# Kernel tuning notes

Measured on AMD Instinct MI355X. Metric: run time of the kernel, lower is better.

## Reference

```python
import jax, jax.numpy as jnp
import numpy as np

N = 50000      # nodes
E = 800000     # edges (undirected, stored once)
D_IN = 128
D_OUT = 128


def setup_inputs() -> dict:
    key = jax.random.key(0)
    k1, k2, k3, k4 = jax.random.split(key, 4)
    X = jax.random.normal(k1, (N, D_IN), dtype=jnp.float32)
    edges = jax.random.randint(k2, (E, 2), 0, N, dtype=jnp.int32)
    weights = jax.random.uniform(k3, (E,), dtype=jnp.float32)
    # glorot_uniform kernel W: [D_IN, D_OUT]
    limit = np.sqrt(6.0 / (D_IN + D_OUT)).astype(np.float32)
    W = jax.random.uniform(k4, (D_IN, D_OUT), dtype=jnp.float32, minval=-limit, maxval=limit)
    return {"X": X, "edges": edges, "weights": weights, "W": W}


def reference(X, edges, weights, W):
    # D^{-1} @ A @ X @ W with A the symmetric weighted adjacency from the edge list.
    # nx.Graph is undirected -> each edge contributes in both directions.
    src = jnp.concatenate([edges[:, 0], edges[:, 1]])   # [2E]
    dst = jnp.concatenate([edges[:, 1], edges[:, 0]])   # [2E]
    w = jnp.concatenate([weights, weights])             # [2E]
    # (A @ X)[i] = sum over edges (j -> i) of w * X[j]
    ax = jax.ops.segment_sum(w[:, None] * X[src], dst, num_segments=N)  # [N, D_IN]
    deg = jax.ops.segment_sum(w, dst, num_segments=N)                   # [N]
    inv_deg = jnp.where(deg > 0, 1.0 / deg, 0.0)                        # D^{-1} (safe for isolated nodes)
    return (ax * inv_deg[:, None]) @ W                                  # [N, D_OUT]
```

## Files before the change

kernel.cpp:

```cpp
#include <hip/hip_runtime.h>
#include <hip/hip_fp16.h>

#define NN 50000
#define NE 800000
#define D  128
#define NB 391
#define NS 256
#define EPS 3125
#define SN (NB * NS)
#define SCB 1024
#define NSB ((SN + SCB - 1) / SCB)

#define OFF_SLAB 0
#define OFF_XW   0
#define OFF_CSR4 12800000
#define OFF_HIST 19200000
#define OFF_BASE 19600384
#define OFF_BSUM 20000768
#define OFF_ROW  20001280
#define OFF_WF   20201344
#define NEED_A   20234112

#define OFF_CNT  0
#define OFF_ROWF 200704
#define OFF_CUR  401408
#define OFF_CSR8 602112

typedef float v2f  __attribute__((ext_vector_type(2)));
typedef __attribute__((ext_vector_type(8))) short bf16x8;
typedef __attribute__((ext_vector_type(4))) float f32x4;

__device__ __forceinline__ float bf_lo(unsigned int v) { return __uint_as_float(v << 16); }
__device__ __forceinline__ float bf_hi(unsigned int v) { return __uint_as_float(v & 0xffff0000u); }
__device__ __forceinline__ float wdec(unsigned int v) {
    return __half2float(__ushort_as_half((unsigned short)(v >> 16)));
}
__device__ __forceinline__ unsigned short bf16rne(float f) {
    unsigned int b = __float_as_uint(f);
    return (unsigned short)((b + 0x7fffu + ((b >> 16) & 1u)) >> 16);
}

__global__ __launch_bounds__(256) void gc_shist(
    const int2* __restrict__ edges, int* __restrict__ histT)
{
    __shared__ int h[NB];
    const int s = blockIdx.x;
    for (int i = threadIdx.x; i < NB; i += 256) h[i] = 0;
    __syncthreads();
    const int e0 = s * EPS;
    for (int i = threadIdx.x; i < EPS; i += 256) {
        int2 p = edges[e0 + i];
        atomicAdd(&h[p.y >> 7], 1);
        atomicAdd(&h[p.x >> 7], 1);
    }
    __syncthreads();
    for (int b = threadIdx.x; b < NB; b += 256) histT[b * NS + s] = h[b];
}

__global__ __launch_bounds__(256) void gc_scanA(
    const int* __restrict__ in, int* __restrict__ bsum)
{
    __shared__ int red[256];
    int base = blockIdx.x * SCB;
    int s = 0;
    for (int i = threadIdx.x; i < SCB; i += 256) {
        int idx = base + i;
        s += (idx < SN) ? in[idx] : 0;
    }
    red[threadIdx.x] = s;
    __syncthreads();
    for (int off = 128; off > 0; off >>= 1) {
        if (threadIdx.x < off) red[threadIdx.x] += red[threadIdx.x + off];
        __syncthreads();
    }
    if (threadIdx.x == 0) bsum[blockIdx.x] = red[0];
}

__global__ __launch_bounds__(256) void gc_scanC(
    const int* __restrict__ in, const int* __restrict__ bsum,
    int* __restrict__ baseT)
{
    __shared__ int part[256];
    __shared__ int sb[128];
    const int t = threadIdx.x;

    int own = 0;
    if (t < 128) {
        own = (t < NSB) ? bsum[t] : 0;
        sb[t] = own;
    }
    __syncthreads();
    for (int off = 1; off < 128; off <<= 1) {
        int v = (t < 128 && t >= off) ? sb[t - off] : 0;
        __syncthreads();
        if (t < 128) sb[t] += v;
        __syncthreads();
    }
    __shared__ int bexc;
    if (t == (int)blockIdx.x) bexc = sb[t] - own;
    __syncthreads();

    int base = blockIdx.x * SCB;
    int idx0 = base + t * 4;
    int4 v = make_int4(0, 0, 0, 0);
    if (idx0 + 3 < SN) v = *reinterpret_cast<const int4*>(in + idx0);
    int s = v.x + v.y + v.z + v.w;
    part[t] = s;
    __syncthreads();
    for (int off = 1; off < 256; off <<= 1) {
        int x = (t >= off) ? part[t - off] : 0;
        __syncthreads();
        part[t] += x;
        __syncthreads();
    }
    int run = bexc + part[t] - s;
    if (idx0 + 3 < SN)
        *reinterpret_cast<int4*>(baseT + idx0) =
            make_int4(run, run + v.x, run + v.x + v.y, run + v.x + v.y + v.z);
}

__global__ __launch_bounds__(256) void gc_sscat(
    const int2* __restrict__ edges, const float* __restrict__ wts,
    const int* __restrict__ baseT, int2* __restrict__ slab)
{
    __shared__ int cur[NB];
    const int s = blockIdx.x;
    for (int b = threadIdx.x; b < NB; b += 256) cur[b] = baseT[b * NS + s];
    __syncthreads();
    const int e0 = s * EPS;
    for (int i = threadIdx.x; i < EPS; i += 256) {
        int2 p = edges[e0 + i];
        int wb = __float_as_int(wts[e0 + i]);
        int b = p.y >> 7;
        int pos = atomicAdd(&cur[b], 1);
        slab[pos] = make_int2(p.x | ((p.y & 127) << 16), wb);
        b = p.x >> 7;
        pos = atomicAdd(&cur[b], 1);
        slab[pos] = make_int2(p.y | ((p.x & 127) << 16), wb);
    }
}

__global__ __launch_bounds__(256) void gc_csr(
    const int* __restrict__ baseT, const int2* __restrict__ slab,
    int* __restrict__ row_start, unsigned int* __restrict__ csr4)
{
    __shared__ int ncnt[128], ncur[128], part[128];
    const int tid = threadIdx.x;
    const int b = blockIdx.x;
    const int start = baseT[b * NS];
    const int end = (b == NB - 1) ? (2 * NE) : baseT[(b + 1) * NS];

    if (tid < 128) ncnt[tid] = 0;
    __syncthreads();

    for (int j = start + tid; j < end; j += 256)
        atomicAdd(&ncnt[(slab[j].x >> 16) & 127], 1);
    __syncthreads();

    if (tid < 128) part[tid] = ncnt[tid];
    __syncthreads();
    for (int off = 1; off < 128; off <<= 1) {
        int v = 0;
        if (tid < 128 && tid >= off) v = part[tid - off];
        __syncthreads();
        if (tid < 128) part[tid] += v;
        __syncthreads();
    }
    if (tid < 128) {
        int st = start + part[tid] - ncnt[tid];
        int n = b * 128 + tid;
        if (n < NN) row_start[n] = st;
        ncur[tid] = st;
    }
    if (b == 0 && tid == 0) row_start[NN] = 2 * NE;
    __syncthreads();

    for (int j = start + tid; j < end; j += 256) {
        int2 en = slab[j];
        int dl = (en.x >> 16) & 127;
        unsigned int hb =
            (unsigned int)__half_as_ushort(__float2half_rn(__int_as_float(en.y))) << 16;
        int pos = atomicAdd(&ncur[dl], 1);
        csr4[pos] = (unsigned int)(en.x & 0xffff) | hb;
    }
}

__global__ __launch_bounds__(256) void gc_wfrag(
    const float* __restrict__ Wm, unsigned short* __restrict__ wf)
{
    int t = blockIdx.x * 256 + threadIdx.x;
    int j    = t & 7;
    int lane = (t >> 3) & 63;
    int nt   = (t >> 9) & 7;
    int ki   = t >> 12;
    int k = ki * 32 + (lane >> 4) * 8 + j;
    int n = nt * 16 + (lane & 15);
    wf[t] = bf16rne(Wm[k * D + n]);
}

__global__ __launch_bounds__(256) void gc_gemm_mfma(
    const float* __restrict__ X, const unsigned short* __restrict__ wf,
    unsigned short* __restrict__ dst)
{
    const int lane = threadIdx.x & 63;
    const int wave = threadIdx.x >> 6;
    const int rbase = blockIdx.x * 64 + wave * 16;
    const int r  = lane & 15;
    const int kb = lane >> 4;

    f32x4 acc[8];
    #pragma unroll
    for (int i = 0; i < 8; ++i) acc[i] = f32x4{0.f, 0.f, 0.f, 0.f};

    const bf16x8* wfv = reinterpret_cast<const bf16x8*>(wf);
    const int row = rbase + r;
    const bool rok = row < NN;

    #pragma unroll
    for (int ki = 0; ki < 4; ++ki) {
        float4 a0 = make_float4(0.f, 0.f, 0.f, 0.f);
        float4 a1 = make_float4(0.f, 0.f, 0.f, 0.f);
        if (rok) {
            const float4* xp = reinterpret_cast<const float4*>(
                X + (size_t)row * D + ki * 32 + kb * 8);
            a0 = xp[0];
            a1 = xp[1];
        }
        bf16x8 af;
        af[0] = (short)bf16rne(a0.x); af[1] = (short)bf16rne(a0.y);
        af[2] = (short)bf16rne(a0.z); af[3] = (short)bf16rne(a0.w);
        af[4] = (short)bf16rne(a1.x); af[5] = (short)bf16rne(a1.y);
        af[6] = (short)bf16rne(a1.z); af[7] = (short)bf16rne(a1.w);
        #pragma unroll
        for (int nt = 0; nt < 8; ++nt) {
            bf16x8 bf = wfv[(ki * 8 + nt) * 64 + lane];
            acc[nt] = __builtin_amdgcn_mfma_f32_16x16x32_bf16(af, bf, acc[nt], 0, 0, 0);
        }
    }

    const int orow0 = rbase + kb * 4;
    #pragma unroll
    for (int nt = 0; nt < 8; ++nt) {
        #pragma unroll
        for (int reg = 0; reg < 4; ++reg) {
            int orow = orow0 + reg;
            if (orow < NN)
                dst[(size_t)orow * D + nt * 16 + r] = bf16rne(acc[nt][reg]);
        }
    }
}

__global__ __launch_bounds__(256) void gc_gather4(
    const int* __restrict__ row_start, const unsigned int* __restrict__ csr4,
    const unsigned int* __restrict__ F, float* __restrict__ out)
{
    int wid  = (blockIdx.x * 256 + threadIdx.x) >> 6;
    unsigned int lane = threadIdx.x & 63;
    if (wid >= NN) return;
    int j   = row_start[wid];
    int end = row_start[wid + 1];
    v2f acc = {0.f, 0.f};
    float dw = 0.f;
    for (; j + 16 <= end; j += 16) {
        unsigned int e[16], v[16];
        #pragma unroll
        for (int q = 0; q < 16; ++q) e[q] = csr4[j + q];
        #pragma unroll
        for (int q = 0; q < 16; ++q) v[q] = F[((e[q] & 0xffffu) << 6) | lane];
        #pragma unroll
        for (int q = 0; q < 16; ++q) {
            float w = wdec(e[q]);
            acc += w * v2f{bf_lo(v[q]), bf_hi(v[q])};
            dw += w;
        }
    }
    for (; j + 4 <= end; j += 4) {
        unsigned int e0 = csr4[j],     e1 = csr4[j + 1];
        unsigned int e2 = csr4[j + 2], e3 = csr4[j + 3];
        unsigned int v0 = F[((e0 & 0xffffu) << 6) | lane];
        unsigned int v1 = F[((e1 & 0xffffu) << 6) | lane];
        unsigned int v2 = F[((e2 & 0xffffu) << 6) | lane];
        unsigned int v3 = F[((e3 & 0xffffu) << 6) | lane];
        float w0 = wdec(e0), w1 = wdec(e1), w2 = wdec(e2), w3 = wdec(e3);
        acc += w0 * v2f{bf_lo(v0), bf_hi(v0)};
        acc += w1 * v2f{bf_lo(v1), bf_hi(v1)};
        acc += w2 * v2f{bf_lo(v2), bf_hi(v2)};
        acc += w3 * v2f{bf_lo(v3), bf_hi(v3)};
        dw += (w0 + w1) + (w2 + w3);
    }
    for (; j < end; ++j) {
        unsigned int e0 = csr4[j];
        unsigned int v0 = F[((e0 & 0xffffu) << 6) | lane];
        float w0 = wdec(e0);
        acc += w0 * v2f{bf_lo(v0), bf_hi(v0)};
        dw += w0;
    }
    float inv = dw > 0.f ? 1.f / dw : 0.f;
    float2 r; r.x = acc.x * inv; r.y = acc.y * inv;
    reinterpret_cast<float2*>(out)[(size_t)wid * 64 + lane] = r;
}

__global__ __launch_bounds__(256) void gc_hist(
    const int2* __restrict__ edges, int* __restrict__ counts)
{
    int e = blockIdx.x * 256 + threadIdx.x;
    if (e >= NE) return;
    int2 p = edges[e];
    atomicAdd(counts + p.x, 1);
    atomicAdd(counts + p.y, 1);
}

__global__ __launch_bounds__(1024) void gc_scan(
    const int* __restrict__ counts, int* __restrict__ row_start,
    int* __restrict__ cursor)
{
    const int CHUNK = (NN + 1023) / 1024;
    __shared__ int part[1024];
    int t = threadIdx.x;
    int lo = t * CHUNK, hi = min(lo + CHUNK, NN);
    int s = 0;
    for (int i = lo; i < hi; ++i) s += counts[i];
    part[t] = s;
    __syncthreads();
    for (int off = 1; off < 1024; off <<= 1) {
        int v = (t >= off) ? part[t - off] : 0;
        __syncthreads();
        part[t] += v;
        __syncthreads();
    }
    int run = part[t] - s;
    for (int i = lo; i < hi; ++i) {
        int c = counts[i];
        row_start[i] = run;
        cursor[i]    = run;
        run += c;
    }
    if (t == 1023) row_start[NN] = part[1023];
}

__global__ __launch_bounds__(256) void gc_fill8(
    const int2* __restrict__ edges, const float* __restrict__ wts,
    int* __restrict__ cursor, int2* __restrict__ csr)
{
    int e = blockIdx.x * 256 + threadIdx.x;
    if (e >= NE) return;
    int2 p = edges[e];
    int wb = __float_as_int(wts[e]);
    int pos = atomicAdd(cursor + p.y, 1);
    csr[pos] = make_int2(p.x, wb);
    pos = atomicAdd(cursor + p.x, 1);
    csr[pos] = make_int2(p.y, wb);
}

__global__ __launch_bounds__(256) void gc_gather_f32(
    const int* __restrict__ row_start, const int2* __restrict__ csr,
    const float* __restrict__ F, float* __restrict__ out)
{
    int wid  = (blockIdx.x * 256 + threadIdx.x) >> 6;
    int lane = threadIdx.x & 63;
    if (wid >= NN) return;
    int j   = row_start[wid];
    int end = row_start[wid + 1];
    const float2* F2 = reinterpret_cast<const float2*>(F);
    float ax = 0.f, ay = 0.f, dw = 0.f;
    for (; j < end; ++j) {
        int2  cw = csr[j];
        float w  = __int_as_float(cw.y);
        float2 xv = F2[(size_t)cw.x * 64 + lane];
        ax = fmaf(w, xv.x, ax);
        ay = fmaf(w, xv.y, ay);
        dw += w;
    }
    float inv = dw > 0.f ? 1.f / dw : 0.f;
    float2 r; r.x = ax * inv; r.y = ay * inv;
    reinterpret_cast<float2*>(out)[(size_t)wid * 64 + lane] = r;
}

__global__ __launch_bounds__(256) void gc_gemm_f32(
    const float* __restrict__ src, float* __restrict__ dst,
    const float* __restrict__ Wm)
{
    __shared__ float Ws[D * D];
    __shared__ float axs[16 * D];
    const int tid = threadIdx.x;
    const int col = tid & 127;
    const int ty  = tid >> 7;
    const int rbase = blockIdx.x * 16;

    const float4* W4  = reinterpret_cast<const float4*>(Wm);
    float4*       Ws4 = reinterpret_cast<float4*>(Ws);
    #pragma unroll
    for (int i = 0; i < 16; ++i) Ws4[tid + i * 256] = W4[tid + i * 256];

    const float4* A4   = reinterpret_cast<const float4*>(src + (size_t)rbase * D);
    float4*       axs4 = reinterpret_cast<float4*>(axs);
    #pragma unroll
    for (int i = 0; i < 2; ++i) axs4[tid + i * 256] = A4[tid + i * 256];
    __syncthreads();

    float acc[8];
    #pragma unroll
    for (int i = 0; i < 8; ++i) acc[i] = 0.f;

    for (int k = 0; k < D; ++k) {
        float wv = Ws[k * D + col];
        #pragma unroll
        for (int i = 0; i < 8; ++i)
            acc[i] = fmaf(axs[(ty * 8 + i) * D + k], wv, acc[i]);
    }

    #pragma unroll
    for (int i = 0; i < 8; ++i)
        dst[(size_t)(rbase + ty * 8 + i) * D + col] = acc[i];
}

extern "C" void kernel_launch(void* const* d_in, const int* in_sizes, int n_in,
                              void* d_out, int out_size, void* d_ws, size_t ws_size,
                              hipStream_t stream) {
    const float* X     = (const float*)d_in[0];
    const int2*  edges = (const int2*)d_in[1];
    const float* wts   = (const float*)d_in[2];
    const float* Wm    = (const float*)d_in[3];
    float* out = (float*)d_out;
    char*  ws  = (char*)d_ws;

    const int eblocks = (NE + 255) / 256;

    if (ws_size >= NEED_A) {
        int2* slab  = (int2*)(ws + OFF_SLAB);
        unsigned int* csr4 = (unsigned int*)(ws + OFF_CSR4);
        int*  histT = (int*)(ws + OFF_HIST);
        int*  baseT = (int*)(ws + OFF_BASE);
        int*  bsum  = (int*)(ws + OFF_BSUM);
        int*  row   = (int*)(ws + OFF_ROW);
        unsigned short* wf = (unsigned short*)(ws + OFF_WF);
        unsigned short* xw = (unsigned short*)(ws + OFF_XW);

        gc_shist<<<NS, 256, 0, stream>>>(edges, histT);
        gc_scanA<<<NSB, 256, 0, stream>>>(histT, bsum);
        gc_scanC<<<NSB, 256, 0, stream>>>(histT, bsum, baseT);
        gc_sscat<<<NS, 256, 0, stream>>>(edges, wts, baseT, slab);
        gc_wfrag<<<64, 256, 0, stream>>>(Wm, wf);
        gc_csr<<<NB, 256, 0, stream>>>(baseT, slab, row, csr4);
        gc_gemm_mfma<<<(NN + 63) / 64, 256, 0, stream>>>(X, wf, xw);
        gc_gather4<<<(NN * 64 + 255) / 256, 256, 0, stream>>>(
            row, csr4, (const unsigned int*)xw, out);
    } else {
        int*  counts    = (int*) (ws + OFF_CNT);
        int*  row_start = (int*) (ws + OFF_ROWF);
        int*  cursor    = (int*) (ws + OFF_CUR);
        int2* csr       = (int2*)(ws + OFF_CSR8);

        hipMemsetAsync(counts, 0, NN * sizeof(int), stream);
        gc_hist<<<eblocks, 256, 0, stream>>>(edges, counts);
        gc_scan<<<1, 1024, 0, stream>>>(counts, row_start, cursor);
        gc_fill8<<<eblocks, 256, 0, stream>>>(edges, wts, cursor, csr);
        gc_gather_f32<<<(NN * 64 + 255) / 256, 256, 0, stream>>>(row_start, csr, X, out);
        gc_gemm_f32<<<NN / 16, 256, 0, stream>>>(out, out, Wm);
    }
}
```

Measured before the change: 108.9 us.

## Fuse CSR build kernels into one cooperative kernel with grid syncs

Merges the six graph-build launches (histogram, two scan phases, scatter, W fragment packing, per-bucket CSR) into a single cooperative kernel of 391 blocks separated by grid-wide barriers. The aim is to remove per-launch overhead and inter-kernel gaps on a short, launch-bound pipeline. The cost is that phases with few active blocks leave most of the grid idle, and each grid.sync adds its own barrier latency. Cooperative launch also needs every block resident at once, which 391 blocks of 256 threads should meet on this GPU.

```diff
diff --git a/kernel.cpp b/kernel.cpp
--- a/kernel.cpp
+++ b/kernel.cpp
@@ -1,5 +1,8 @@
 #include <hip/hip_runtime.h>
 #include <hip/hip_fp16.h>
+#include <hip/hip_cooperative_groups.h>
+
+namespace cg = cooperative_groups;
 
 #define NN 50000
 #define NE 800000
@@ -40,162 +43,157 @@
     return (unsigned short)((b + 0x7fffu + ((b >> 16) & 1u)) >> 16);
 }
 
-__global__ __launch_bounds__(256) void gc_shist(
-    const int2* __restrict__ edges, int* __restrict__ histT)
-{
+__global__ __launch_bounds__(256) void gc_build(
+    const int2* __restrict__ edges, const float* __restrict__ wts,
+    const float* __restrict__ Wm, int* __restrict__ histT,
+    int* __restrict__ bsum, int* __restrict__ baseT,
+    int2* __restrict__ slab, int* __restrict__ row_start,
+    unsigned int* __restrict__ csr4, unsigned short* __restrict__ wf)
+{
+    cg::grid_group grid = cg::this_grid();
     __shared__ int h[NB];
-    const int s = blockIdx.x;
-    for (int i = threadIdx.x; i < NB; i += 256) h[i] = 0;
-    __syncthreads();
-    const int e0 = s * EPS;
-    for (int i = threadIdx.x; i < EPS; i += 256) {
-        int2 p = edges[e0 + i];
-        atomicAdd(&h[p.y >> 7], 1);
-        atomicAdd(&h[p.x >> 7], 1);
-    }
-    __syncthreads();
-    for (int b = threadIdx.x; b < NB; b += 256) histT[b * NS + s] = h[b];
-}
-
-__global__ __launch_bounds__(256) void gc_scanA(
-    const int* __restrict__ in, int* __restrict__ bsum)
-{
-    __shared__ int red[256];
-    int base = blockIdx.x * SCB;
-    int s = 0;
-    for (int i = threadIdx.x; i < SCB; i += 256) {
-        int idx = base + i;
-        s += (idx < SN) ? in[idx] : 0;
-    }
-    red[threadIdx.x] = s;
-    __syncthreads();
-    for (int off = 128; off > 0; off >>= 1) {
-        if (threadIdx.x < off) red[threadIdx.x] += red[threadIdx.x + off];
-        __syncthreads();
-    }
-    if (threadIdx.x == 0) bsum[blockIdx.x] = red[0];
-}
-
-__global__ __launch_bounds__(256) void gc_scanC(
-    const int* __restrict__ in, const int* __restrict__ bsum,
-    int* __restrict__ baseT)
-{
     __shared__ int part[256];
     __shared__ int sb[128];
-    const int t = threadIdx.x;
-
-    int own = 0;
-    if (t < 128) {
-        own = (t < NSB) ? bsum[t] : 0;
-        sb[t] = own;
-    }
-    __syncthreads();
-    for (int off = 1; off < 128; off <<= 1) {
-        int v = (t < 128 && t >= off) ? sb[t - off] : 0;
-        __syncthreads();
-        if (t < 128) sb[t] += v;
-        __syncthreads();
-    }
-    __shared__ int bexc;
-    if (t == (int)blockIdx.x) bexc = sb[t] - own;
-    __syncthreads();
-
-    int base = blockIdx.x * SCB;
-    int idx0 = base + t * 4;
-    int4 v = make_int4(0, 0, 0, 0);
-    if (idx0 + 3 < SN) v = *reinterpret_cast<const int4*>(in + idx0);
-    int s = v.x + v.y + v.z + v.w;
-    part[t] = s;
-    __syncthreads();
-    for (int off = 1; off < 256; off <<= 1) {
-        int x = (t >= off) ? part[t - off] : 0;
-        __syncthreads();
-        part[t] += x;
-        __syncthreads();
-    }
-    int run = bexc + part[t] - s;
-    if (idx0 + 3 < SN)
-        *reinterpret_cast<int4*>(baseT + idx0) =
-            make_int4(run, run + v.x, run + v.x + v.y, run + v.x + v.y + v.z);
-}
-
-__global__ __launch_bounds__(256) void gc_sscat(
-    const int2* __restrict__ edges, const float* __restrict__ wts,
-    const int* __restrict__ baseT, int2* __restrict__ slab)
-{
-    __shared__ int cur[NB];
-    const int s = blockIdx.x;
-    for (int b = threadIdx.x; b < NB; b += 256) cur[b] = baseT[b * NS + s];
-    __syncthreads();
-    const int e0 = s * EPS;
-    for (int i = threadIdx.x; i < EPS; i += 256) {
-        int2 p = edges[e0 + i];
-        int wb = __float_as_int(wts[e0 + i]);
-        int b = p.y >> 7;
-        int pos = atomicAdd(&cur[b], 1);
-        slab[pos] = make_int2(p.x | ((p.y & 127) << 16), wb);
-        b = p.x >> 7;
-        pos = atomicAdd(&cur[b], 1);
-        slab[pos] = make_int2(p.y | ((p.x & 127) << 16), wb);
-    }
-}
-
-__global__ __launch_bounds__(256) void gc_csr(
-    const int* __restrict__ baseT, const int2* __restrict__ slab,
-    int* __restrict__ row_start, unsigned int* __restrict__ csr4)
-{
-    __shared__ int ncnt[128], ncur[128], part[128];
+    __shared__ int bexc_s;
+    __shared__ int ncnt[128], ncur[128];
+
     const int tid = threadIdx.x;
-    const int b = blockIdx.x;
-    const int start = baseT[b * NS];
-    const int end = (b == NB - 1) ? (2 * NE) : baseT[(b + 1) * NS];
-
-    if (tid < 128) ncnt[tid] = 0;
-    __syncthreads();
-
-    for (int j = start + tid; j < end; j += 256)
-        atomicAdd(&ncnt[(slab[j].x >> 16) & 127], 1);
-    __syncthreads();
-
-    if (tid < 128) part[tid] = ncnt[tid];
-    __syncthreads();
-    for (int off = 1; off < 128; off <<= 1) {
-        int v = 0;
-        if (tid < 128 && tid >= off) v = part[tid - off];
-        __syncthreads();
-        if (tid < 128) part[tid] += v;
-        __syncthreads();
-    }
-    if (tid < 128) {
-        int st = start + part[tid] - ncnt[tid];
-        int n = b * 128 + tid;
-        if (n < NN) row_start[n] = st;
-        ncur[tid] = st;
-    }
-    if (b == 0 && tid == 0) row_start[NN] = 2 * NE;
-    __syncthreads();
-
-    for (int j = start + tid; j < end; j += 256) {
-        int2 en = slab[j];
-        int dl = (en.x >> 16) & 127;
-        unsigned int hb =
-            (unsigned int)__half_as_ushort(__float2half_rn(__int_as_float(en.y))) << 16;
-        int pos = atomicAdd(&ncur[dl], 1);
-        csr4[pos] = (unsigned int)(en.x & 0xffff) | hb;
-    }
-}
-
-__global__ __launch_bounds__(256) void gc_wfrag(
-    const float* __restrict__ Wm, unsigned short* __restrict__ wf)
-{
-    int t = blockIdx.x * 256 + threadIdx.x;
-    int j    = t & 7;
-    int lane = (t >> 3) & 63;
-    int nt   = (t >> 9) & 7;
-    int ki   = t >> 12;
-    int k = ki * 32 + (lane >> 4) * 8 + j;
-    int n = nt * 16 + (lane & 15);
-    wf[t] = bf16rne(Wm[k * D + n]);
+    const int bid = blockIdx.x;
+
+    if (bid < NS) {
+        const int s = bid;
+        for (int i = tid; i < NB; i += 256) h[i] = 0;
+        __syncthreads();
+        const int e0 = s * EPS;
+        for (int i = tid; i < EPS; i += 256) {
+            int2 p = edges[e0 + i];
+            atomicAdd(&h[p.y >> 7], 1);
+            atomicAdd(&h[p.x >> 7], 1);
+        }
+        __syncthreads();
+        for (int b = tid; b < NB; b += 256) histT[b * NS + s] = h[b];
+    } else if (bid < NS + 64) {
+        int t = (bid - NS) * 256 + tid;
+        int j    = t & 7;
+        int lane = (t >> 3) & 63;
+        int nt   = (t >> 9) & 7;
+        int ki   = t >> 12;
+        int k = ki * 32 + (lane >> 4) * 8 + j;
+        int n = nt * 16 + (lane & 15);
+        wf[t] = bf16rne(Wm[k * D + n]);
+    }
+    grid.sync();
+
+    if (bid < NSB) {
+        int base = bid * SCB;
+        int s = 0;
+        for (int i = tid; i < SCB; i += 256) {
+            int idx = base + i;
+            s += (idx < SN) ? histT[idx] : 0;
+        }
+        part[tid] = s;
+        __syncthreads();
+        for (int off = 128; off > 0; off >>= 1) {
+            if (tid < off) part[tid] += part[tid + off];
+            __syncthreads();
+        }
+        if (tid == 0) bsum[bid] = part[0];
+    }
+    grid.sync();
+
+    if (bid < NSB) {
+        int own = 0;
+        if (tid < 128) {
+            own = (tid < NSB) ? bsum[tid] : 0;
+            sb[tid] = own;
+        }
+        __syncthreads();
+        for (int off = 1; off < 128; off <<= 1) {
+            int v = (tid < 128 && tid >= off) ? sb[tid - off] : 0;
+            __syncthreads();
+            if (tid < 128) sb[tid] += v;
+            __syncthreads();
+        }
+        if (tid == bid) bexc_s = sb[tid] - own;
+        __syncthreads();
+
+        int base = bid * SCB;
+        int idx0 = base + tid * 4;
+        int4 v = make_int4(0, 0, 0, 0);
+        if (idx0 + 3 < SN) v = *reinterpret_cast<const int4*>(histT + idx0);
+        int s = v.x + v.y + v.z + v.w;
+        part[tid] = s;
+        __syncthreads();
+        for (int off = 1; off < 256; off <<= 1) {
+            int x = (tid >= off) ? part[tid - off] : 0;
+            __syncthreads();
+            part[tid] += x;
+            __syncthreads();
+        }
+        int run = bexc_s + part[tid] - s;
+        if (idx0 + 3 < SN)
+            *reinterpret_cast<int4*>(baseT + idx0) =
+                make_int4(run, run + v.x, run + v.x + v.y, run + v.x + v.y + v.z);
+    }
+    grid.sync();
+
+    if (bid < NS) {
+        const int s = bid;
+        for (int b = tid; b < NB; b += 256) h[b] = baseT[b * NS + s];
+        __syncthreads();
+        const int e0 = s * EPS;
+        for (int i = tid; i < EPS; i += 256) {
+            int2 p = edges[e0 + i];
+            int wb = __float_as_int(wts[e0 + i]);
+            int b = p.y >> 7;
+            int pos = atomicAdd(&h[b], 1);
+            slab[pos] = make_int2(p.x | ((p.y & 127) << 16), wb);
+            b = p.x >> 7;
+            pos = atomicAdd(&h[b], 1);
+            slab[pos] = make_int2(p.y | ((p.x & 127) << 16), wb);
+        }
+    }
+    grid.sync();
+
+    {
+        const int b = bid;
+        const int start = baseT[b * NS];
+        const int end = (b == NB - 1) ? (2 * NE) : baseT[(b + 1) * NS];
+
+        if (tid < 128) ncnt[tid] = 0;
+        __syncthreads();
+
+        for (int j = start + tid; j < end; j += 256)
+            atomicAdd(&ncnt[(slab[j].x >> 16) & 127], 1);
+        __syncthreads();
+
+        if (tid < 128) part[tid] = ncnt[tid];
+        __syncthreads();
+        for (int off = 1; off < 128; off <<= 1) {
+            int v = 0;
+            if (tid < 128 && tid >= off) v = part[tid - off];
+            __syncthreads();
+            if (tid < 128) part[tid] += v;
+            __syncthreads();
+        }
+        if (tid < 128) {
+            int st = start + part[tid] - ncnt[tid];
+            int n = b * 128 + tid;
+            if (n < NN) row_start[n] = st;
+            ncur[tid] = st;
+        }
+        if (b == 0 && tid == 0) row_start[NN] = 2 * NE;
+        __syncthreads();
+
+        for (int j = start + tid; j < end; j += 256) {
+            int2 en = slab[j];
+            int dl = (en.x >> 16) & 127;
+            unsigned int hb =
+                (unsigned int)__half_as_ushort(__float2half_rn(__int_as_float(en.y))) << 16;
+            int pos = atomicAdd(&ncur[dl], 1);
+            csr4[pos] = (unsigned int)(en.x & 0xffff) | hb;
+        }
+    }
 }
 
 __global__ __launch_bounds__(256) void gc_gemm_mfma(
@@ -436,12 +434,13 @@
         unsigned short* wf = (unsigned short*)(ws + OFF_WF);
         unsigned short* xw = (unsigned short*)(ws + OFF_XW);
 
-        gc_shist<<<NS, 256, 0, stream>>>(edges, histT);
-        gc_scanA<<<NSB, 256, 0, stream>>>(histT, bsum);
-        gc_scanC<<<NSB, 256, 0, stream>>>(histT, bsum, baseT);
-        gc_sscat<<<NS, 256, 0, stream>>>(edges, wts, baseT, slab);
-        gc_wfrag<<<64, 256, 0, stream>>>(Wm, wf);
-        gc_csr<<<NB, 256, 0, stream>>>(baseT, slab, row, csr4);
+        void* args[] = {
+            (void*)&edges, (void*)&wts, (void*)&Wm, (void*)&histT,
+            (void*)&bsum, (void*)&baseT, (void*)&slab, (void*)&row,
+            (void*)&csr4, (void*)&wf
+        };
+        hipLaunchCooperativeKernel((void*)gc_build, dim3(NB), dim3(256),
+                                   args, 0, stream);
         gc_gemm_mfma<<<(NN + 63) / 64, 256, 0, stream>>>(X, wf, xw);
         gc_gather4<<<(NN * 64 + 255) / 256, 256, 0, stream>>>(
             row, csr4, (const unsigned int*)xw, out);
```

New measurement: 296.4 us. 2.72x slower.

## Replace two-pass scan with decoupled look-back scan and fuse wfrag into histogram

Applied to the files above, without the earlier changes.

Replaces the reduce-then-scan pair of kernels with a single-pass scan that chains block prefixes through flagged descriptors (decoupled look-back). The W-to-bf16 fragment conversion and the descriptor zeroing are folded into the histogram launch as extra blocks. This cuts two kernel launches and their serialization gaps, at the cost of spin-waiting on relaxed atomics, which depends on earlier blocks being scheduled first.

```diff
diff --git a/kernel.cpp b/kernel.cpp
--- a/kernel.cpp
+++ b/kernel.cpp
@@ -11,12 +11,15 @@
 #define SCB 1024
 #define NSB ((SN + SCB - 1) / SCB)
 
+#define FLAG_PART 0x40000000u
+#define FLAG_INC  0x80000000u
+
 #define OFF_SLAB 0
 #define OFF_XW   0
 #define OFF_CSR4 12800000
 #define OFF_HIST 19200000
 #define OFF_BASE 19600384
-#define OFF_BSUM 20000768
+#define OFF_DESC 20000768
 #define OFF_ROW  20001280
 #define OFF_WF   20201344
 #define NEED_A   20234112
@@ -41,69 +44,50 @@
 }
 
 __global__ __launch_bounds__(256) void gc_shist(
-    const int2* __restrict__ edges, int* __restrict__ histT)
-{
-    __shared__ int h[NB];
-    const int s = blockIdx.x;
-    for (int i = threadIdx.x; i < NB; i += 256) h[i] = 0;
-    __syncthreads();
-    const int e0 = s * EPS;
-    for (int i = threadIdx.x; i < EPS; i += 256) {
-        int2 p = edges[e0 + i];
-        atomicAdd(&h[p.y >> 7], 1);
-        atomicAdd(&h[p.x >> 7], 1);
-    }
-    __syncthreads();
-    for (int b = threadIdx.x; b < NB; b += 256) histT[b * NS + s] = h[b];
-}
-
-__global__ __launch_bounds__(256) void gc_scanA(
-    const int* __restrict__ in, int* __restrict__ bsum)
-{
-    __shared__ int red[256];
-    int base = blockIdx.x * SCB;
-    int s = 0;
-    for (int i = threadIdx.x; i < SCB; i += 256) {
-        int idx = base + i;
-        s += (idx < SN) ? in[idx] : 0;
-    }
-    red[threadIdx.x] = s;
-    __syncthreads();
-    for (int off = 128; off > 0; off >>= 1) {
-        if (threadIdx.x < off) red[threadIdx.x] += red[threadIdx.x + off];
-        __syncthreads();
-    }
-    if (threadIdx.x == 0) bsum[blockIdx.x] = red[0];
-}
-
-__global__ __launch_bounds__(256) void gc_scanC(
-    const int* __restrict__ in, const int* __restrict__ bsum,
+    const int2* __restrict__ edges, int* __restrict__ histT,
+    const float* __restrict__ Wm, unsigned short* __restrict__ wf,
+    unsigned int* __restrict__ desc)
+{
+    const int bid = blockIdx.x;
+    const int tid = threadIdx.x;
+    if (bid < NS) {
+        __shared__ int h[NB];
+        for (int i = tid; i < NB; i += 256) h[i] = 0;
+        __syncthreads();
+        const int e0 = bid * EPS;
+        for (int i = tid; i < EPS; i += 256) {
+            int2 p = edges[e0 + i];
+            atomicAdd(&h[p.y >> 7], 1);
+            atomicAdd(&h[p.x >> 7], 1);
+        }
+        __syncthreads();
+        for (int b = tid; b < NB; b += 256) histT[b * NS + bid] = h[b];
+    } else if (bid < NS + 64) {
+        int t = (bid - NS) * 256 + tid;
+        int j    = t & 7;
+        int lane = (t >> 3) & 63;
+        int nt   = (t >> 9) & 7;
+        int ki   = t >> 12;
+        int k = ki * 32 + (lane >> 4) * 8 + j;
+        int n = nt * 16 + (lane & 15);
+        wf[t] = bf16rne(Wm[k * D + n]);
+    } else {
+        if (tid < NSB) desc[tid] = 0u;
+    }
+}
+
+__global__ __launch_bounds__(256) void gc_scan1(
+    const int* __restrict__ histT, unsigned int* __restrict__ desc,
     int* __restrict__ baseT)
 {
     __shared__ int part[256];
-    __shared__ int sb[128];
+    __shared__ int bexc_sh;
     const int t = threadIdx.x;
-
-    int own = 0;
-    if (t < 128) {
-        own = (t < NSB) ? bsum[t] : 0;
-        sb[t] = own;
-    }
-    __syncthreads();
-    for (int off = 1; off < 128; off <<= 1) {
-        int v = (t < 128 && t >= off) ? sb[t - off] : 0;
-        __syncthreads();
-        if (t < 128) sb[t] += v;
-        __syncthreads();
-    }
-    __shared__ int bexc;
-    if (t == (int)blockIdx.x) bexc = sb[t] - own;
-    __syncthreads();
-
-    int base = blockIdx.x * SCB;
+    const int b = blockIdx.x;
+    int base = b * SCB;
     int idx0 = base + t * 4;
     int4 v = make_int4(0, 0, 0, 0);
-    if (idx0 + 3 < SN) v = *reinterpret_cast<const int4*>(in + idx0);
+    if (idx0 + 3 < SN) v = *reinterpret_cast<const int4*>(histT + idx0);
     int s = v.x + v.y + v.z + v.w;
     part[t] = s;
     __syncthreads();
@@ -113,7 +97,32 @@
         part[t] += x;
         __syncthreads();
     }
-    int run = bexc + part[t] - s;
+    if (t == 0) {
+        int agg = part[255];
+        if (b == 0) {
+            __hip_atomic_store(&desc[0], FLAG_INC | (unsigned)agg,
+                               __ATOMIC_RELAXED, __HIP_MEMORY_SCOPE_AGENT);
+            bexc_sh = 0;
+        } else {
+            __hip_atomic_store(&desc[b], FLAG_PART | (unsigned)agg,
+                               __ATOMIC_RELAXED, __HIP_MEMORY_SCOPE_AGENT);
+            int run = 0;
+            int j = b - 1;
+            while (true) {
+                unsigned d = __hip_atomic_load(&desc[j], __ATOMIC_RELAXED,
+                                               __HIP_MEMORY_SCOPE_AGENT);
+                if (d == 0u) continue;
+                run += (int)(d & 0x3FFFFFFFu);
+                if (d & FLAG_INC) break;
+                --j;
+            }
+            bexc_sh = run;
+            __hip_atomic_store(&desc[b], FLAG_INC | (unsigned)(run + agg),
+                               __ATOMIC_RELAXED, __HIP_MEMORY_SCOPE_AGENT);
+        }
+    }
+    __syncthreads();
+    int run = bexc_sh + part[t] - s;
     if (idx0 + 3 < SN)
         *reinterpret_cast<int4*>(baseT + idx0) =
             make_int4(run, run + v.x, run + v.x + v.y, run + v.x + v.y + v.z);
@@ -183,19 +192,6 @@
         int pos = atomicAdd(&ncur[dl], 1);
         csr4[pos] = (unsigned int)(en.x & 0xffff) | hb;
     }
-}
-
-__global__ __launch_bounds__(256) void gc_wfrag(
-    const float* __restrict__ Wm, unsigned short* __restrict__ wf)
-{
-    int t = blockIdx.x * 256 + threadIdx.x;
-    int j    = t & 7;
-    int lane = (t >> 3) & 63;
-    int nt   = (t >> 9) & 7;
-    int ki   = t >> 12;
-    int k = ki * 32 + (lane >> 4) * 8 + j;
-    int n = nt * 16 + (lane & 15);
-    wf[t] = bf16rne(Wm[k * D + n]);
 }
 
 __global__ __launch_bounds__(256) void gc_gemm_mfma(
@@ -431,16 +427,14 @@
         unsigned int* csr4 = (unsigned int*)(ws + OFF_CSR4);
         int*  histT = (int*)(ws + OFF_HIST);
         int*  baseT = (int*)(ws + OFF_BASE);
-        int*  bsum  = (int*)(ws + OFF_BSUM);
+        unsigned int* desc = (unsigned int*)(ws + OFF_DESC);
         int*  row   = (int*)(ws + OFF_ROW);
         unsigned short* wf = (unsigned short*)(ws + OFF_WF);
         unsigned short* xw = (unsigned short*)(ws + OFF_XW);
 
-        gc_shist<<<NS, 256, 0, stream>>>(edges, histT);
-        gc_scanA<<<NSB, 256, 0, stream>>>(histT, bsum);
-        gc_scanC<<<NSB, 256, 0, stream>>>(histT, bsum, baseT);
+        gc_shist<<<NS + 64 + 1, 256, 0, stream>>>(edges, histT, Wm, wf, desc);
+        gc_scan1<<<NSB, 256, 0, stream>>>(histT, desc, baseT);
         gc_sscat<<<NS, 256, 0, stream>>>(edges, wts, baseT, slab);
-        gc_wfrag<<<64, 256, 0, stream>>>(Wm, wf);
         gc_csr<<<NB, 256, 0, stream>>>(baseT, slab, row, csr4);
         gc_gemm_mfma<<<(NN + 63) / 64, 256, 0, stream>>>(X, wf, xw);
         gc_gather4<<<(NN * 64 + 255) / 256, 256, 0, stream>>>(
```

After: 112.0 us. 1.03x slower.

## Merge W-fragment prep into histogram and GEMM into scatter kernel launches

Applied to the files above, without the earlier changes.

Folds the W-to-bf16 fragment conversion into the histogram kernel as extra blocks, and runs the X@W MFMA GEMM as extra blocks of the edge-scatter kernel. This removes two kernel launches and lets the GEMM overlap the latency-bound scatter instead of running after CSR build. Because the slab and xw buffers are now live at the same time, xw gets its own workspace region, which raises the workspace requirement and could select the fallback path if the workspace is too small.

```diff
diff --git a/kernel.cpp b/kernel.cpp
--- a/kernel.cpp
+++ b/kernel.cpp
@@ -10,16 +10,17 @@
 #define SN (NB * NS)
 #define SCB 1024
 #define NSB ((SN + SCB - 1) / SCB)
+#define GEMMB ((NN + 63) / 64)
 
 #define OFF_SLAB 0
-#define OFF_XW   0
 #define OFF_CSR4 12800000
 #define OFF_HIST 19200000
 #define OFF_BASE 19600384
 #define OFF_BSUM 20000768
 #define OFF_ROW  20001280
 #define OFF_WF   20201344
-#define NEED_A   20234112
+#define OFF_XW   20234112
+#define NEED_A   33034112
 
 #define OFF_CNT  0
 #define OFF_ROWF 200704
@@ -41,20 +42,33 @@
 }
 
 __global__ __launch_bounds__(256) void gc_shist(
-    const int2* __restrict__ edges, int* __restrict__ histT)
-{
-    __shared__ int h[NB];
-    const int s = blockIdx.x;
-    for (int i = threadIdx.x; i < NB; i += 256) h[i] = 0;
-    __syncthreads();
-    const int e0 = s * EPS;
-    for (int i = threadIdx.x; i < EPS; i += 256) {
-        int2 p = edges[e0 + i];
-        atomicAdd(&h[p.y >> 7], 1);
-        atomicAdd(&h[p.x >> 7], 1);
-    }
-    __syncthreads();
-    for (int b = threadIdx.x; b < NB; b += 256) histT[b * NS + s] = h[b];
+    const int2* __restrict__ edges, int* __restrict__ histT,
+    const float* __restrict__ Wm, unsigned short* __restrict__ wf)
+{
+    const int bid = blockIdx.x;
+    const int tid = threadIdx.x;
+    if (bid < NS) {
+        __shared__ int h[NB];
+        for (int i = tid; i < NB; i += 256) h[i] = 0;
+        __syncthreads();
+        const int e0 = bid * EPS;
+        for (int i = tid; i < EPS; i += 256) {
+            int2 p = edges[e0 + i];
+            atomicAdd(&h[p.y >> 7], 1);
+            atomicAdd(&h[p.x >> 7], 1);
+        }
+        __syncthreads();
+        for (int b = tid; b < NB; b += 256) histT[b * NS + bid] = h[b];
+    } else if (bid < NS + 64) {
+        int t = (bid - NS) * 256 + tid;
+        int j    = t & 7;
+        int lane = (t >> 3) & 63;
+        int nt   = (t >> 9) & 7;
+        int ki   = t >> 12;
+        int k = ki * 32 + (lane >> 4) * 8 + j;
+        int n = nt * 16 + (lane & 15);
+        wf[t] = bf16rne(Wm[k * D + n]);
+    }
 }
 
 __global__ __launch_bounds__(256) void gc_scanA(
@@ -82,6 +96,7 @@
 {
     __shared__ int part[256];
     __shared__ int sb[128];
+    __shared__ int bexc;
     const int t = threadIdx.x;
 
     int own = 0;
@@ -96,7 +111,6 @@
         if (t < 128) sb[t] += v;
         __syncthreads();
     }
-    __shared__ int bexc;
     if (t == (int)blockIdx.x) bexc = sb[t] - own;
     __syncthreads();
 
@@ -119,24 +133,78 @@
             make_int4(run, run + v.x, run + v.x + v.y, run + v.x + v.y + v.z);
 }
 
-__global__ __launch_bounds__(256) void gc_sscat(
+__global__ __launch_bounds__(256) void gc_sscat_gemm(
     const int2* __restrict__ edges, const float* __restrict__ wts,
-    const int* __restrict__ baseT, int2* __restrict__ slab)
-{
-    __shared__ int cur[NB];
-    const int s = blockIdx.x;
-    for (int b = threadIdx.x; b < NB; b += 256) cur[b] = baseT[b * NS + s];
-    __syncthreads();
-    const int e0 = s * EPS;
-    for (int i = threadIdx.x; i < EPS; i += 256) {
-        int2 p = edges[e0 + i];
-        int wb = __float_as_int(wts[e0 + i]);
-        int b = p.y >> 7;
-        int pos = atomicAdd(&cur[b], 1);
-        slab[pos] = make_int2(p.x | ((p.y & 127) << 16), wb);
-        b = p.x >> 7;
-        pos = atomicAdd(&cur[b], 1);
-        slab[pos] = make_int2(p.y | ((p.x & 127) << 16), wb);
+    const int* __restrict__ baseT, int2* __restrict__ slab,
+    const float* __restrict__ X, const unsigned short* __restrict__ wf,
+    unsigned short* __restrict__ xw)
+{
+    const int bid = blockIdx.x;
+    const int tid = threadIdx.x;
+    if (bid < NS) {
+        __shared__ int cur[NB];
+        const int s = bid;
+        for (int b = tid; b < NB; b += 256) cur[b] = baseT[b * NS + s];
+        __syncthreads();
+        const int e0 = s * EPS;
+        for (int i = tid; i < EPS; i += 256) {
+            int2 p = edges[e0 + i];
+            int wb = __float_as_int(wts[e0 + i]);
+            int b = p.y >> 7;
+            int pos = atomicAdd(&cur[b], 1);
+            slab[pos] = make_int2(p.x | ((p.y & 127) << 16), wb);
+            b = p.x >> 7;
+            pos = atomicAdd(&cur[b], 1);
+            slab[pos] = make_int2(p.y | ((p.x & 127) << 16), wb);
+        }
+    } else {
+        const int gb   = bid - NS;
+        const int lane = tid & 63;
+        const int wave = tid >> 6;
+        const int rbase = gb * 64 + wave * 16;
+        const int r  = lane & 15;
+        const int kb = lane >> 4;
+
+        f32x4 acc[8];
+        #pragma unroll
+        for (int i = 0; i < 8; ++i) acc[i] = f32x4{0.f, 0.f, 0.f, 0.f};
+
+        const bf16x8* wfv = reinterpret_cast<const bf16x8*>(wf);
+        const int row = rbase + r;
+        const bool rok = row < NN;
+
+        #pragma unroll
+        for (int ki = 0; ki < 4; ++ki) {
+            float4 a0 = make_float4(0.f, 0.f, 0.f, 0.f);
+            float4 a1 = make_float4(0.f, 0.f, 0.f, 0.f);
+            if (rok) {
+                const float4* xp = reinterpret_cast<const float4*>(
+                    X + (size_t)row * D + ki * 32 + kb * 8);
+                a0 = xp[0];
+                a1 = xp[1];
+            }
+            bf16x8 af;
+            af[0] = (short)bf16rne(a0.x); af[1] = (short)bf16rne(a0.y);
+            af[2] = (short)bf16rne(a0.z); af[3] = (short)bf16rne(a0.w);
+            af[4] = (short)bf16rne(a1.x); af[5] = (short)bf16rne(a1.y);
+            af[6] = (short)bf16rne(a1.z); af[7] = (short)bf16rne(a1.w);
+            #pragma unroll
+            for (int nt = 0; nt < 8; ++nt) {
+                bf16x8 bf = wfv[(ki * 8 + nt) * 64 + lane];
+                acc[nt] = __builtin_amdgcn_mfma_f32_16x16x32_bf16(af, bf, acc[nt], 0, 0, 0);
+            }
+        }
+
+        const int orow0 = rbase + kb * 4;
+        #pragma unroll
+        for (int nt = 0; nt < 8; ++nt) {
+            #pragma unroll
+            for (int reg = 0; reg < 4; ++reg) {
+                int orow = orow0 + reg;
+                if (orow < NN)
+                    xw[(size_t)orow * D + nt * 16 + r] = bf16rne(acc[nt][reg]);
+            }
+        }
     }
 }
 
@@ -182,71 +250,6 @@
             (unsigned int)__half_as_ushort(__float2half_rn(__int_as_float(en.y))) << 16;
         int pos = atomicAdd(&ncur[dl], 1);
         csr4[pos] = (unsigned int)(en.x & 0xffff) | hb;
-    }
-}
-
-__global__ __launch_bounds__(256) void gc_wfrag(
-    const float* __restrict__ Wm, unsigned short* __restrict__ wf)
-{
-    int t = blockIdx.x * 256 + threadIdx.x;
-    int j    = t & 7;
-    int lane = (t >> 3) & 63;
-    int nt   = (t >> 9) & 7;
-    int ki   = t >> 12;
-    int k = ki * 32 + (lane >> 4) * 8 + j;
-    int n = nt * 16 + (lane & 15);
-    wf[t] = bf16rne(Wm[k * D + n]);
-}
-
-__global__ __launch_bounds__(256) void gc_gemm_mfma(
-    const float* __restrict__ X, const unsigned short* __restrict__ wf,
-    unsigned short* __restrict__ dst)
-{
-    const int lane = threadIdx.x & 63;
-    const int wave = threadIdx.x >> 6;
-    const int rbase = blockIdx.x * 64 + wave * 16;
-    const int r  = lane & 15;
-    const int kb = lane >> 4;
-
-    f32x4 acc[8];
-    #pragma unroll
-    for (int i = 0; i < 8; ++i) acc[i] = f32x4{0.f, 0.f, 0.f, 0.f};
-
-    const bf16x8* wfv = reinterpret_cast<const bf16x8*>(wf);
-    const int row = rbase + r;
-    const bool rok = row < NN;
-
-    #pragma unroll
-    for (int ki = 0; ki < 4; ++ki) {
-        float4 a0 = make_float4(0.f, 0.f, 0.f, 0.f);
-        float4 a1 = make_float4(0.f, 0.f, 0.f, 0.f);
-        if (rok) {
-            const float4* xp = reinterpret_cast<const float4*>(
-                X + (size_t)row * D + ki * 32 + kb * 8);
-            a0 = xp[0];
-            a1 = xp[1];
-        }
-        bf16x8 af;
-        af[0] = (short)bf16rne(a0.x); af[1] = (short)bf16rne(a0.y);
-        af[2] = (short)bf16rne(a0.z); af[3] = (short)bf16rne(a0.w);
-        af[4] = (short)bf16rne(a1.x); af[5] = (short)bf16rne(a1.y);
-        af[6] = (short)bf16rne(a1.z); af[7] = (short)bf16rne(a1.w);
-        #pragma unroll
-        for (int nt = 0; nt < 8; ++nt) {
-            bf16x8 bf = wfv[(ki * 8 + nt) * 64 + lane];
-            acc[nt] = __builtin_amdgcn_mfma_f32_16x16x32_bf16(af, bf, acc[nt], 0, 0, 0);
-        }
-    }
-
-    const int orow0 = rbase + kb * 4;
-    #pragma unroll
-    for (int nt = 0; nt < 8; ++nt) {
-        #pragma unroll
-        for (int reg = 0; reg < 4; ++reg) {
-            int orow = orow0 + reg;
-            if (orow < NN)
-                dst[(size_t)orow * D + nt * 16 + r] = bf16rne(acc[nt][reg]);
-        }
     }
 }
 
@@ -436,13 +439,12 @@
         unsigned short* wf = (unsigned short*)(ws + OFF_WF);
         unsigned short* xw = (unsigned short*)(ws + OFF_XW);
 
-        gc_shist<<<NS, 256, 0, stream>>>(edges, histT);
+        gc_shist<<<NS + 64, 256, 0, stream>>>(edges, histT, Wm, wf);
         gc_scanA<<<NSB, 256, 0, stream>>>(histT, bsum);
         gc_scanC<<<NSB, 256, 0, stream>>>(histT, bsum, baseT);
-        gc_sscat<<<NS, 256, 0, stream>>>(edges, wts, baseT, slab);
-        gc_wfrag<<<64, 256, 0, stream>>>(Wm, wf);
+        gc_sscat_gemm<<<NS + GEMMB, 256, 0, stream>>>(
+            edges, wts, baseT, slab, X, wf, xw);
         gc_csr<<<NB, 256, 0, stream>>>(baseT, slab, row, csr4);
-        gc_gemm_mfma<<<(NN + 63) / 64, 256, 0, stream>>>(X, wf, xw);
         gc_gather4<<<(NN * 64 + 255) / 256, 256, 0, stream>>>(
             row, csr4, (const unsigned int*)xw, out);
     } else {
```

After: 102.0 us. 1.07x faster.
